# Performance work log

Hardware: AMD Instinct MI355X
Metric: run time of the kernel (lower is better)

## Reference

```python
import jax, jax.numpy as jnp
import numpy as np

CUT_SIZE = 224  # cut_size init arg
CUTN = 32       # cutn init arg
CUT_POW = 1.0


def setup_inputs() -> dict:
    key = jax.random.key(0)
    B, C, H, W = 16, 3, 512, 512
    x = jax.random.normal(key, (B, C, H, W), dtype=jnp.float32)
    # Replicate the module's host-side RNG: size = rand()**cut_pow*(max-min)+min,
    # offset = randint(0, side - size + 1). Generated with numpy for determinism.
    rs = np.random.RandomState(0)
    max_size = min(H, W)
    min_size = min(H, W, CUT_SIZE)
    sizes = (rs.rand(CUTN) ** CUT_POW * (max_size - min_size) + min_size).astype(np.int32)
    offsetx = np.floor(rs.rand(CUTN) * (W - sizes + 1)).astype(np.int32)
    offsety = np.floor(rs.rand(CUTN) * (H - sizes + 1)).astype(np.int32)
    return {
        "x": x,
        "sizes": jnp.asarray(sizes),
        "offsetx": jnp.asarray(offsetx),
        "offsety": jnp.asarray(offsety),
    }


def reference(x, sizes, offsetx, offsety):
    # x: [B, C, H, W]; sizes/offsetx/offsety: [cutn] int32
    B, C, H, W = x.shape
    i = jnp.arange(CUT_SIZE, dtype=jnp.int32)
    # PyTorch F.interpolate default 'nearest': src = floor(out_idx * in/out)
    yidx = offsety[:, None] + (i[None, :] * sizes[:, None]) // CUT_SIZE  # [cutn, cut]
    xidx = offsetx[:, None] + (i[None, :] * sizes[:, None]) // CUT_SIZE  # [cutn, cut]
    # Fused crop + nearest-resize for all cutouts via one batched gather
    out = x[:, :, yidx[:, :, None], xidx[:, None, :]]  # [B, C, cutn, cut, cut]
    out = jnp.transpose(out, (2, 0, 1, 3, 4))           # [cutn, B, C, cut, cut]
    return out.reshape(CUTN * B, C, CUT_SIZE, CUT_SIZE)  # matches th.cat over cutn
```

## Files before the change

### kernel.cpp

```cpp
#include <hip/hip_runtime.h>


#define CUT_SIZE 224
#define CUTN     32
#define BATCH    16
#define CHAN     3
#define HEIGHT   512
#define WIDTH    512
#define J4       (CUT_SIZE / 4)

__global__ __launch_bounds__(256) void make_cutouts_kernel(
    const float* __restrict__ x,
    const int*   __restrict__ sizes,
    const int*   __restrict__ offsetx,
    const int*   __restrict__ offsety,
    float4*      __restrict__ out,
    int total_vec4)
{
    int v = blockIdx.x * blockDim.x + threadIdx.x;
    if (v >= total_vec4) return;

    int j4 = v % J4;
    int t  = v / J4;
    int i  = t % CUT_SIZE;
    t /= CUT_SIZE;
    int c  = t % CHAN;
    t /= CHAN;
    int b  = t % BATCH;
    int n  = t / BATCH;

    const int sz = sizes[n];
    const int ox = offsetx[n];
    const int oy = offsety[n];

    const int yy = oy + (i * sz) / CUT_SIZE;
    const int j0 = j4 * 4;
    const int x0 = ox + ((j0 + 0) * sz) / CUT_SIZE;
    const int x1 = ox + ((j0 + 1) * sz) / CUT_SIZE;
    const int x2 = ox + ((j0 + 2) * sz) / CUT_SIZE;
    const int x3 = ox + ((j0 + 3) * sz) / CUT_SIZE;

    const float* __restrict__ row =
        x + ((size_t)((b * CHAN + c) * HEIGHT + yy)) * WIDTH;

    float4 r;
    r.x = row[x0];
    r.y = row[x1];
    r.z = row[x2];
    r.w = row[x3];
    out[v] = r;
}

extern "C" void kernel_launch(void* const* d_in, const int* in_sizes, int n_in,
                              void* d_out, int out_size, void* d_ws, size_t ws_size,
                              hipStream_t stream) {
    const float* x       = (const float*)d_in[0];
    const int*   sizes   = (const int*)d_in[1];
    const int*   offsetx = (const int*)d_in[2];
    const int*   offsety = (const int*)d_in[3];
    float4*      out     = (float4*)d_out;

    const int total_vec4 = CUTN * BATCH * CHAN * CUT_SIZE * J4;
    const int block = 256;
    const int grid  = (total_vec4 + block - 1) / block;

    make_cutouts_kernel<<<grid, block, 0, stream>>>(x, sizes, offsetx, offsety,
                                                    out, total_vec4);
}
```

Baseline: 405.8 us.

## Stage selected source rows in LDS and gather columns from shared memory

Result: slower. 416.7 us (+2.7%).

```diff
diff --git a/kernel.cpp b/kernel.cpp
--- a/kernel.cpp
+++ b/kernel.cpp
@@ -7,48 +7,54 @@
 #define CHAN     3
 #define HEIGHT   512
 #define WIDTH    512
-#define J4       (CUT_SIZE / 4)
+#define R_       8
+#define CHUNKS   (CUT_SIZE / R_)
+#define PLANES   (BATCH * CHAN)
 
-__global__ __launch_bounds__(256) void make_cutouts_kernel(
+__global__ __launch_bounds__(256, 8) void make_cutouts_kernel(
     const float* __restrict__ x,
     const int*   __restrict__ sizes,
     const int*   __restrict__ offsetx,
     const int*   __restrict__ offsety,
-    float4*      __restrict__ out,
-    int total_vec4)
+    float*       __restrict__ out)
 {
-    int v = blockIdx.x * blockDim.x + threadIdx.x;
-    if (v >= total_vec4) return;
+    __shared__ float smem[R_ * WIDTH];
 
-    int j4 = v % J4;
-    int t  = v / J4;
-    int i  = t % CUT_SIZE;
-    t /= CUT_SIZE;
-    int c  = t % CHAN;
-    t /= CHAN;
-    int b  = t % BATCH;
-    int n  = t / BATCH;
+    const int bid   = blockIdx.x;
+    const int chunk = bid % CHUNKS;
+    const int t2    = bid / CHUNKS;
+    const int bc    = t2 % PLANES;
+    const int n     = t2 / PLANES;
 
     const int sz = sizes[n];
     const int ox = offsetx[n];
     const int oy = offsety[n];
+    const int i0 = chunk * R_;
 
-    const int yy = oy + (i * sz) / CUT_SIZE;
-    const int j0 = j4 * 4;
-    const int x0 = ox + ((j0 + 0) * sz) / CUT_SIZE;
-    const int x1 = ox + ((j0 + 1) * sz) / CUT_SIZE;
-    const int x2 = ox + ((j0 + 2) * sz) / CUT_SIZE;
-    const int x3 = ox + ((j0 + 3) * sz) / CUT_SIZE;
+    const int tid = threadIdx.x;
 
-    const float* __restrict__ row =
-        x + ((size_t)((b * CHAN + c) * HEIGHT + yy)) * WIDTH;
+    const float4* plane = (const float4*)(x + (size_t)bc * (HEIGHT * WIDTH));
+    float4* s4 = (float4*)smem;
+    #pragma unroll
+    for (int k = 0; k < (R_ * (WIDTH / 4)) / 256; ++k) {
+        const int idx = tid + k * 256;
+        const int r   = idx >> 7;
+        const int c4  = idx & 127;
+        const int yy  = oy + ((i0 + r) * sz) / CUT_SIZE;
+        s4[r * (WIDTH / 4) + c4] = plane[yy * (WIDTH / 4) + c4];
+    }
+    __syncthreads();
 
-    float4 r;
-    r.x = row[x0];
-    r.y = row[x1];
-    r.z = row[x2];
-    r.w = row[x3];
-    out[v] = r;
+    if (tid < CUT_SIZE) {
+        const int j  = tid;
+        const int xc = ox + (j * sz) / CUT_SIZE;
+        float* o = out + (size_t)(n * PLANES + bc) * (CUT_SIZE * CUT_SIZE)
+                       + (size_t)i0 * CUT_SIZE + j;
+        #pragma unroll
+        for (int r = 0; r < R_; ++r) {
+            o[r * CUT_SIZE] = smem[r * WIDTH + xc];
+        }
+    }
 }
 
 extern "C" void kernel_launch(void* const* d_in, const int* in_sizes, int n_in,
@@ -58,12 +64,8 @@
     const int*   sizes   = (const int*)d_in[1];
     const int*   offsetx = (const int*)d_in[2];
     const int*   offsety = (const int*)d_in[3];
-    float4*      out     = (float4*)d_out;
+    float*       out     = (float*)d_out;
 
-    const int total_vec4 = CUTN * BATCH * CHAN * CUT_SIZE * J4;
-    const int block = 256;
-    const int grid  = (total_vec4 + block - 1) / block;
-
-    make_cutouts_kernel<<<grid, block, 0, stream>>>(x, sizes, offsetx, offsety,
-                                                    out, total_vec4);
+    const int grid = CUTN * PLANES * CHUNKS;
+    make_cutouts_kernel<<<grid, 256, 0, stream>>>(x, sizes, offsetx, offsety, out);
 }
```
